# Performance work log

Measured on AMD Instinct MI355X. Metric: run time of the kernel, lower is better.

The kernel has to match this reference:

```python
import jax, jax.numpy as jnp
import numpy as np

N_USERS = 100000
N_ITEMS = 50000
N_NODES = N_USERS + N_ITEMS
N_EDGES = 4800000
EMB_DIM = 64
N_LAYERS = 3


def setup_inputs() -> dict:
    key = jax.random.key(0)
    k1, k2, k3, k4, k5 = jax.random.split(key, 5)
    adj_rows = jax.random.randint(k1, (N_EDGES,), 0, N_NODES, dtype=jnp.int64 if jax.config.jax_enable_x64 else jnp.int32)
    adj_cols = jax.random.randint(k2, (N_EDGES,), 0, N_NODES, dtype=jnp.int64 if jax.config.jax_enable_x64 else jnp.int32)
    adj_vals = jax.random.uniform(k3, (N_EDGES,), dtype=jnp.float32)
    user_emb = jax.random.normal(k4, (N_USERS, EMB_DIM), dtype=jnp.float32)
    item_emb = jax.random.normal(k5, (N_ITEMS, EMB_DIM), dtype=jnp.float32)
    return {"adj_rows": adj_rows, "adj_cols": adj_cols, "adj_vals": adj_vals,
            "user_emb": user_emb, "item_emb": item_emb}


def _spmm(rows, cols, vals, x):
    # sparse.mm(adj, x): gather source node features, scale by edge value,
    # scatter-add into destination rows. Shapes: [E] indices, [N, D] features.
    msgs = vals[:, None] * x[cols]          # [E, D]
    return jax.ops.segment_sum(msgs, rows, num_segments=N_NODES)  # [N, D]


def reference(adj_rows, adj_cols, adj_vals, user_emb, item_emb):
    all_emb = jnp.concatenate([user_emb, item_emb], axis=0)  # [N, D]
    acc = all_emb                                            # running sum over layers (fused stack+mean)
    emb = all_emb
    for _ in range(N_LAYERS):
        emb = _spmm(adj_rows, adj_cols, adj_vals, emb)
        acc = acc + emb
    final = acc / jnp.asarray(N_LAYERS + 1, dtype=acc.dtype)
    return final[:N_USERS], final[N_USERS:]
```

## Files before the change

### kernel.cpp

```cpp
#include <hip/hip_runtime.h>


#define N_USERS 100000
#define N_ITEMS 50000
#define N_NODES 150000
#define N_EDGES 4800000
#define EMB_DIM 64

typedef unsigned short u16;
typedef unsigned int   u32;

constexpr int NODE_FLOATS  = N_NODES * EMB_DIM;
constexpr int NODE_FLOAT4S = NODE_FLOATS / 4;
constexpr int USER_FLOAT4S = N_USERS * EMB_DIM / 4;

constexpr int NB   = (N_NODES + 255) / 256;
constexpr int NXG  = 8;
constexpr int SEG  = NB * NXG;
constexpr int CAP1 = 1280;
constexpr int EPB  = 6144;
constexpr int ABLK2 = (N_EDGES + EPB - 1) / EPB;
constexpr int SB_CAP2 = 10880;
constexpr int CSR_CAP = 6000000;

static __device__ __forceinline__ float bf2f(u16 b) {
    return __uint_as_float(((u32)b) << 16);
}
static __device__ __forceinline__ u16 f2bf(float f) {
    u32 u = __float_as_uint(f);
    return (u16)((u + 0x7FFFu + ((u >> 16) & 1u)) >> 16);
}

__global__ void init_kernel(const float* __restrict__ user_emb,
                            const float* __restrict__ item_emb,
                            u16* __restrict__ emb) {
    int i = blockIdx.x * blockDim.x + threadIdx.x;
    if (i >= NODE_FLOAT4S) return;
    float4 v = (i < USER_FLOAT4S) ? ((const float4*)user_emb)[i]
                                  : ((const float4*)item_emb)[i - USER_FLOAT4S];
    ushort4 o;
    o.x = f2bf(v.x); o.y = f2bf(v.y); o.z = f2bf(v.z); o.w = f2bf(v.w);
    ((ushort4*)emb)[i] = o;
}

__global__ void init_ptrs_kernel(int* __restrict__ bx_pos, int* __restrict__ csr_cursor) {
    int i = blockIdx.x * blockDim.x + threadIdx.x;
    if (i < SEG) bx_pos[i * 16] = i * CAP1;
    if (i == 0) csr_cursor[0] = 0;
}

__global__ void stageA2_kernel(const int* __restrict__ rows,
                               const int* __restrict__ cols,
                               const float* __restrict__ vals,
                               int* __restrict__ bx_pos,
                               u32* __restrict__ stage_key,
                               u16* __restrict__ stage_val) {
    __shared__ u32 lkey[EPB];
    __shared__ u16 lval[EPB];
    __shared__ u16 lbkt[EPB];
    __shared__ int hist[NB];
    __shared__ int hstart[NB];
    __shared__ int hcur[NB];
    __shared__ int gbase[NB];
    __shared__ int ws4[4];

    const int tid  = threadIdx.x;
    const int base = blockIdx.x * EPB;
    const int cnt  = min(EPB, N_EDGES - base);
    const int x    = blockIdx.x & (NXG - 1);

    for (int i = tid; i < NB; i += 256) hist[i] = 0;
    __syncthreads();

    for (int k = 0; k < EPB / 256; k += 8) {
        int rbuf[8];
        #pragma unroll
        for (int q = 0; q < 8; ++q) {
            int idx = (k + q) * 256 + tid;
            rbuf[q] = (idx < cnt) ? rows[base + idx] : -1;
        }
        #pragma unroll
        for (int q = 0; q < 8; ++q)
            if (rbuf[q] >= 0) atomicAdd(&hist[rbuf[q] >> 8], 1);
    }
    __syncthreads();

    const int lane = tid & 63, wave = tid >> 6;
    int carry = 0;
    for (int c0 = 0; c0 < NB; c0 += 256) {
        int i = c0 + tid;
        int v = (i < NB) ? hist[i] : 0;
        int incl = v;
        #pragma unroll
        for (int off = 1; off < 64; off <<= 1) {
            int t = __shfl_up(incl, off);
            if (lane >= off) incl += t;
        }
        if (lane == 63) ws4[wave] = incl;
        __syncthreads();
        int wpref = 0, tot = 0;
        #pragma unroll
        for (int w = 0; w < 4; ++w) { int s = ws4[w]; if (w < wave) wpref += s; tot += s; }
        int excl = carry + wpref + incl - v;
        if (i < NB) { hstart[i] = excl; hcur[i] = excl; }
        carry += tot;
        __syncthreads();
    }

    for (int k = 0; k < EPB / 256; k += 8) {
        int rb[8], cb[8]; float vb[8];
        #pragma unroll
        for (int q = 0; q < 8; ++q) {
            int idx = (k + q) * 256 + tid;
            if (idx < cnt) { rb[q] = rows[base + idx]; cb[q] = cols[base + idx]; vb[q] = vals[base + idx]; }
            else rb[q] = -1;
        }
        #pragma unroll
        for (int q = 0; q < 8; ++q) {
            if (rb[q] < 0) continue;
            int b = rb[q] >> 8;
            int p = atomicAdd(&hcur[b], 1);
            lkey[p] = ((u32)(rb[q] & 255) << 24) | (u32)cb[q];
            lval[p] = f2bf(vb[q]);
            lbkt[p] = (u16)b;
        }
    }
    __syncthreads();

    for (int i = tid; i < NB; i += 256) {
        int n = hist[i];
        if (n) {
            int seg = i * NXG + x;
            int p = atomicAdd(&bx_pos[seg * 16], n);
            gbase[i] = (p + n <= (seg + 1) * CAP1) ? p : -1;
        }
    }
    __syncthreads();

    for (int i = tid; i < cnt; i += 256) {
        int b  = lbkt[i];
        int gb = gbase[b];
        if (gb >= 0) {
            int d = gb + (i - hstart[b]);
            stage_key[d] = lkey[i];
            stage_val[d] = lval[i];
        }
    }
}

__global__ void stageB2_kernel(const int* __restrict__ bx_pos,
                               const u32* __restrict__ stage_key,
                               const u16* __restrict__ stage_val,
                               int* __restrict__ csr_cursor,
                               u32* __restrict__ csr_col,
                               u16* __restrict__ csr_val,
                               u32* __restrict__ desc) {
    __shared__ u32 skey[SB_CAP2];
    __shared__ u16 sval[SB_CAP2];
    __shared__ int rhist[256], rpad0[256], rcur[256];
    __shared__ int ws4[4];
    __shared__ int sbase_sh;

    const int b   = blockIdx.x;
    const int tid = threadIdx.x;
    rhist[tid] = 0;
    __syncthreads();

    for (int xx = 0; xx < NXG; ++xx) {
        int seg = b * NXG + xx;
        int sb  = seg * CAP1;
        int n   = min(bx_pos[seg * 16] - sb, CAP1);
        for (int i = tid; i < n; i += 256)
            atomicAdd(&rhist[stage_key[sb + i] >> 24], 1);
    }
    __syncthreads();

    const int lane = tid & 63, wave = tid >> 6;
    int v  = rhist[tid];
    int vp = (v + 15) & ~15;
    int incl = vp;
    #pragma unroll
    for (int off = 1; off < 64; off <<= 1) {
        int t = __shfl_up(incl, off);
        if (lane >= off) incl += t;
    }
    if (lane == 63) ws4[wave] = incl;
    __syncthreads();
    int wpref = 0, total = 0;
    #pragma unroll
    for (int w = 0; w < 4; ++w) { int s = ws4[w]; if (w < wave) wpref += s; total += s; }
    int excl = wpref + incl - vp;
    rpad0[tid] = excl;
    rcur[tid]  = excl;
    if (tid == 0) sbase_sh = atomicAdd(csr_cursor, total);
    __syncthreads();

    const int tcap = min(total, SB_CAP2);
    for (int i = tid; i < tcap; i += 256) { skey[i] = 0u; sval[i] = 0; }
    __syncthreads();

    for (int xx = 0; xx < NXG; ++xx) {
        int seg = b * NXG + xx;
        int sb  = seg * CAP1;
        int n   = min(bx_pos[seg * 16] - sb, CAP1);
        for (int i = tid; i < n; i += 256) {
            u32 key = stage_key[sb + i];
            u16 val = stage_val[sb + i];
            int p = atomicAdd(&rcur[key >> 24], 1);
            if (p < SB_CAP2) { skey[p] = key & 0x00FFFFFFu; sval[p] = val; }
        }
    }
    __syncthreads();

    const int sbase = sbase_sh;
    for (int i = tid; i < tcap; i += 256) {
        int g = sbase + i;
        if (g < CSR_CAP) { csr_col[g] = skey[i]; csr_val[g] = sval[i]; }
    }
    int grow = b * 256 + tid;
    if (grow < N_NODES) {
        int cp = vp; if (cp > 240) cp = 240;
        desc[grow] = ((u32)(sbase + rpad0[tid]) << 8) | (u32)cp;
    }
}

__global__ __launch_bounds__(256, 8)
void spmm_rw_kernel(const u32* __restrict__ desc,
                    const u32* __restrict__ csr_col,
                    const u16* __restrict__ csr_val,
                    const u16* __restrict__ x,
                    u16* __restrict__ y,
                    const u16* __restrict__ e0,
                    const u16* __restrict__ y1,
                    const u16* __restrict__ y2,
                    float* __restrict__ out) {
    const int lane = threadIdx.x & 63;
    const int wid  = __builtin_amdgcn_readfirstlane(threadIdx.x >> 6);
    const int row  = blockIdx.x * 4 + wid;
    if (row >= N_NODES) return;

    const u32 d   = desc[row];
    const int beg = (int)(d >> 8);
    const int nch = (int)(d & 255u) >> 4;

    const u32* __restrict__ pc = csr_col + beg;
    const u32* __restrict__ pv = ((const u32*)csr_val) + (beg >> 1);
    const u16* __restrict__ xl = x + lane;

    float a[4] = {0.f, 0.f, 0.f, 0.f};

    for (int ch = 0; ch < nch; ++ch) {
        u32 c[16];
        u32 w[8];
        #pragma unroll
        for (int k = 0; k < 16; ++k) c[k] = pc[ch * 16 + k];
        #pragma unroll
        for (int k = 0; k < 8; ++k)  w[k] = pv[ch * 8 + k];

        u32 xv[16];
        #pragma unroll
        for (int k = 0; k < 16; ++k)
            xv[k] = (u32)xl[(size_t)c[k] * EMB_DIM];

        #pragma unroll
        for (int k = 0; k < 16; ++k) {
            u32 vb = (k & 1) ? (w[k >> 1] & 0xFFFF0000u) : (w[k >> 1] << 16);
            float vv = __uint_as_float(vb);
            float xf = __uint_as_float(xv[k] << 16);
            a[k & 3] += vv * xf;
        }
    }
    float s = (a[0] + a[1]) + (a[2] + a[3]);

    size_t oidx = (size_t)row * EMB_DIM + lane;
    if (y) {
        y[oidx] = f2bf(s);
    } else {
        float r = (bf2f(e0[oidx]) + bf2f(y1[oidx]) + bf2f(y2[oidx]) + s) * 0.25f;
        out[oidx] = r;
    }
}

__global__ void init3_kernel(const float* __restrict__ user_emb,
                             const float* __restrict__ item_emb,
                             float* __restrict__ emb,
                             float* __restrict__ acc,
                             float* __restrict__ nxt) {
    int i = blockIdx.x * blockDim.x + threadIdx.x;
    if (i >= NODE_FLOAT4S) return;
    float4 v = (i < USER_FLOAT4S) ? ((const float4*)user_emb)[i]
                                  : ((const float4*)item_emb)[i - USER_FLOAT4S];
    ((float4*)emb)[i] = v;
    ((float4*)acc)[i] = v;
    ((float4*)nxt)[i] = make_float4(0.f, 0.f, 0.f, 0.f);
}

__global__ void spmm_atomic_kernel(const int* __restrict__ rows,
                                   const int* __restrict__ cols,
                                   const float* __restrict__ vals,
                                   const float* __restrict__ x,
                                   float* __restrict__ y) {
    unsigned tid = blockIdx.x * blockDim.x + threadIdx.x;
    unsigned e  = tid >> 4;
    unsigned d4 = tid & 15u;
    if (e >= N_EDGES) return;
    int r = rows[e]; int c = cols[e]; float v = vals[e];
    float4 xv = ((const float4*)(x + (size_t)c * EMB_DIM))[d4];
    float* yp = y + (size_t)r * EMB_DIM + d4 * 4;
    atomicAdd(yp + 0, v * xv.x);
    atomicAdd(yp + 1, v * xv.y);
    atomicAdd(yp + 2, v * xv.z);
    atomicAdd(yp + 3, v * xv.w);
}

__global__ void acc_kernel(float* __restrict__ acc, const float* __restrict__ nxt,
                           float* __restrict__ zbuf, int do_zero, float scale) {
    int i = blockIdx.x * blockDim.x + threadIdx.x;
    if (i >= NODE_FLOAT4S) return;
    float4 a = ((float4*)acc)[i];
    float4 n = ((const float4*)nxt)[i];
    a.x = (a.x + n.x) * scale; a.y = (a.y + n.y) * scale;
    a.z = (a.z + n.z) * scale; a.w = (a.w + n.w) * scale;
    ((float4*)acc)[i] = a;
    if (do_zero) ((float4*)zbuf)[i] = make_float4(0.f, 0.f, 0.f, 0.f);
}

extern "C" void kernel_launch(void* const* d_in, const int* in_sizes, int n_in,
                              void* d_out, int out_size, void* d_ws, size_t ws_size,
                              hipStream_t stream) {
    const int*   rows     = (const int*)d_in[0];
    const int*   cols     = (const int*)d_in[1];
    const float* vals     = (const float*)d_in[2];
    const float* user_emb = (const float*)d_in[3];
    const float* item_emb = (const float*)d_in[4];
    float* out = (float*)d_out;

    constexpr size_t U_BUF   = (size_t)NODE_FLOATS / 2;
    constexpr size_t U_SKEY  = (size_t)SEG * CAP1;
    constexpr size_t U_SVAL  = U_SKEY / 2;
    constexpr size_t U_STAGE = 2 * U_BUF;
    constexpr size_t U_CCOL  = (size_t)CSR_CAP;
    constexpr size_t U_CVAL  = (size_t)CSR_CAP / 2;
    size_t need_u32 = U_BUF + U_STAGE + U_CCOL + U_CVAL + (size_t)N_NODES
                    + (size_t)SEG * 16 + 16;

    const int EW_BLOCKS = (NODE_FLOAT4S + 255) / 256;

    if (ws_size >= need_u32 * 4) {
        u32* W = (u32*)d_ws;
        u16* buf0      = (u16*)W;
        u32* stage_key = W + U_BUF;
        u16* stage_val = (u16*)(W + U_BUF + U_SKEY);
        u16* buf1      = (u16*)(W + U_BUF);
        u16* buf2      = (u16*)(W + U_BUF + U_BUF);
        u32* csr_col   = W + U_BUF + U_STAGE;
        u16* csr_val   = (u16*)(csr_col + U_CCOL);
        u32* desc      = (u32*)(csr_col + U_CCOL + U_CVAL);
        int* bx_pos    = (int*)(desc + N_NODES);
        int* csr_cur   = bx_pos + (size_t)SEG * 16;

        init_ptrs_kernel<<<(SEG + 255) / 256, 256, 0, stream>>>(bx_pos, csr_cur);
        init_kernel<<<EW_BLOCKS, 256, 0, stream>>>(user_emb, item_emb, buf0);
        stageA2_kernel<<<ABLK2, 256, 0, stream>>>(rows, cols, vals, bx_pos,
                                                  stage_key, stage_val);
        stageB2_kernel<<<NB, 256, 0, stream>>>(bx_pos, stage_key, stage_val,
                                               csr_cur, csr_col, csr_val, desc);

        const int SPMM_BLOCKS = (N_NODES + 3) / 4;
        spmm_rw_kernel<<<SPMM_BLOCKS, 256, 0, stream>>>(desc, csr_col, csr_val,
                                                        buf0, buf1, nullptr, nullptr, nullptr, nullptr);
        spmm_rw_kernel<<<SPMM_BLOCKS, 256, 0, stream>>>(desc, csr_col, csr_val,
                                                        buf1, buf2, nullptr, nullptr, nullptr, nullptr);
        spmm_rw_kernel<<<SPMM_BLOCKS, 256, 0, stream>>>(desc, csr_col, csr_val,
                                                        buf2, nullptr, buf0, buf1, buf2, out);
    } else {
        float* buf0 = (float*)d_ws;
        float* buf1 = buf0 + NODE_FLOATS;
        const int SPMM_BLOCKS = (int)(((size_t)N_EDGES * 16 + 255) / 256);
        init3_kernel<<<EW_BLOCKS, 256, 0, stream>>>(user_emb, item_emb, buf0, out, buf1);
        float* prev = buf0; float* next = buf1;
        for (int layer = 0; layer < 3; ++layer) {
            spmm_atomic_kernel<<<SPMM_BLOCKS, 256, 0, stream>>>(rows, cols, vals, prev, next);
            if (layer < 2) acc_kernel<<<EW_BLOCKS, 256, 0, stream>>>(out, next, prev, 1, 1.0f);
            else           acc_kernel<<<EW_BLOCKS, 256, 0, stream>>>(out, next, prev, 0, 0.25f);
            float* t = prev; prev = next; next = t;
        }
    }
}
```

Measured before the change: 489.1 us.

## Double-buffer SpMM gather loads with manual vmcnt waits and scalar CSR indices

Restructures the row-per-wavefront SpMM loop into a two-stage software pipeline. The next 16-edge chunk's feature gathers are issued through inline-asm global_load_ushort before the current chunk is accumulated, and explicit s_waitcnt vmcnt plus sched barriers sequence the two stages. Row start and chunk count are forced wave-uniform with readfirstlane so the CSR column and value reads can become scalar loads. Occupancy bounds are lowered from 8 to 6 to make room for the extra registers. Manual waitcnt bookkeeping is fragile if the compiler emits other vector loads inside the window.

```diff
diff --git a/kernel.cpp b/kernel.cpp
--- a/kernel.cpp
+++ b/kernel.cpp
@@ -224,7 +224,40 @@
     }
 }
 
-__global__ __launch_bounds__(256, 8)
+
+static __device__ __forceinline__ void issue16(u32 (&bx)[16], u32 (&bw)[8],
+                                               const u32* __restrict__ pc,
+                                               const u32* __restrict__ pv,
+                                               int ch, u32 lane2,
+                                               const u16* __restrict__ x) {
+    #pragma unroll
+    for (int k = 0; k < 8; ++k) bw[k] = pv[ch * 8 + k];
+    #pragma unroll
+    for (int k = 0; k < 16; ++k) {
+        u32 off = (pc[ch * 16 + k] << 7) + lane2;
+        asm volatile("global_load_ushort %0, %1, %2"
+                     : "=v"(bx[k])
+                     : "v"(off), "s"(x)
+                     : "memory");
+    }
+}
+
+static __device__ __forceinline__ void fma16(const u32 (&bx)[16], const u32 (&bw)[8],
+                                             float (&a)[4]) {
+    #pragma unroll
+    for (int k = 0; k < 16; ++k) {
+        u32 w  = bw[k >> 1];
+        u32 vb = (k & 1) ? (w & 0xFFFF0000u) : (w << 16);
+        a[k & 3] += __uint_as_float(vb) * __uint_as_float(bx[k] << 16);
+    }
+}
+
+#define SPMM_WAIT_PIPE  { asm volatile("s_waitcnt vmcnt(16)" ::: "memory"); \
+                          __builtin_amdgcn_sched_barrier(0); }
+#define SPMM_WAIT_ALL   { asm volatile("s_waitcnt vmcnt(0)" ::: "memory");  \
+                          __builtin_amdgcn_sched_barrier(0); }
+
+__global__ __launch_bounds__(256, 6)
 void spmm_rw_kernel(const u32* __restrict__ desc,
                     const u32* __restrict__ csr_col,
                     const u16* __restrict__ csr_val,
@@ -235,39 +268,33 @@
                     const u16* __restrict__ y2,
                     float* __restrict__ out) {
     const int lane = threadIdx.x & 63;
+    const u32 lane2 = (u32)lane * 2u;
     const int wid  = __builtin_amdgcn_readfirstlane(threadIdx.x >> 6);
     const int row  = blockIdx.x * 4 + wid;
     if (row >= N_NODES) return;
 
     const u32 d   = desc[row];
-    const int beg = (int)(d >> 8);
-    const int nch = (int)(d & 255u) >> 4;
+    const int beg = __builtin_amdgcn_readfirstlane((int)(d >> 8));
+    const int nch = __builtin_amdgcn_readfirstlane((int)(d & 255u) >> 4);
 
     const u32* __restrict__ pc = csr_col + beg;
     const u32* __restrict__ pv = ((const u32*)csr_val) + (beg >> 1);
-    const u16* __restrict__ xl = x + lane;
 
     float a[4] = {0.f, 0.f, 0.f, 0.f};
-
-    for (int ch = 0; ch < nch; ++ch) {
-        u32 c[16];
-        u32 w[8];
-        #pragma unroll
-        for (int k = 0; k < 16; ++k) c[k] = pc[ch * 16 + k];
-        #pragma unroll
-        for (int k = 0; k < 8; ++k)  w[k] = pv[ch * 8 + k];
-
-        u32 xv[16];
-        #pragma unroll
-        for (int k = 0; k < 16; ++k)
-            xv[k] = (u32)xl[(size_t)c[k] * EMB_DIM];
-
-        #pragma unroll
-        for (int k = 0; k < 16; ++k) {
-            u32 vb = (k & 1) ? (w[k >> 1] & 0xFFFF0000u) : (w[k >> 1] << 16);
-            float vv = __uint_as_float(vb);
-            float xf = __uint_as_float(xv[k] << 16);
-            a[k & 3] += vv * xf;
+    u32 Ax[16], Aw[8], Bx[16], Bw[8];
+
+    if (nch > 0) {
+        issue16(Ax, Aw, pc, pv, 0, lane2, x);
+        int ch = 0;
+        for (;;) {
+            if (ch + 1 < nch) { issue16(Bx, Bw, pc, pv, ch + 1, lane2, x); SPMM_WAIT_PIPE; }
+            else              { SPMM_WAIT_ALL; }
+            fma16(Ax, Aw, a);
+            if (++ch >= nch) break;
+            if (ch + 1 < nch) { issue16(Ax, Aw, pc, pv, ch + 1, lane2, x); SPMM_WAIT_PIPE; }
+            else              { SPMM_WAIT_ALL; }
+            fma16(Bx, Bw, a);
+            if (++ch >= nch) break;
         }
     }
     float s = (a[0] + a[1]) + (a[2] + a[3]);
@@ -337,7 +364,6 @@
 
     constexpr size_t U_BUF   = (size_t)NODE_FLOATS / 2;
     constexpr size_t U_SKEY  = (size_t)SEG * CAP1;
-    constexpr size_t U_SVAL  = U_SKEY / 2;
     constexpr size_t U_STAGE = 2 * U_BUF;
     constexpr size_t U_CCOL  = (size_t)CSR_CAP;
     constexpr size_t U_CVAL  = (size_t)CSR_CAP / 2;
```

Measured after the change: 981.2 us. +100.6%, slower.
